# Kernel optimization log

Hardware: AMD Instinct MI355X
Metric: run time of the kernel (lower is better)

The kernel has to match this reference:

```python
import jax, jax.numpy as jnp
import numpy as np

CLASS_W, MASK_W, DICE_W = 1.0, 1.0, 1.0
BIG = 1.0e6


def _hungarian_np(cost):
    """Jonker-Volgenant style shortest-augmenting-path Hungarian (same optimum as
    scipy.optimize.linear_sum_assignment). cost: [R, C] numpy. Returns (row_ind, col_ind)
    with row_ind sorted ascending."""
    C = np.asarray(cost, dtype=np.float64)
    transposed = C.shape[0] > C.shape[1]
    if transposed:
        C = C.T
    n, m = C.shape  # n <= m
    u = np.zeros(n + 1)
    v = np.zeros(m + 1)
    p = np.zeros(m + 1, dtype=np.int64)   # p[j] = row (1-based) matched to col j
    way = np.zeros(m + 1, dtype=np.int64)
    for i in range(1, n + 1):
        p[0] = i
        j0 = 0
        minv = np.full(m + 1, np.inf)
        used = np.zeros(m + 1, dtype=bool)
        while True:
            used[j0] = True
            i0 = p[j0]
            free = ~used
            free[0] = False
            js = np.nonzero(free)[0]
            cur = C[i0 - 1, js - 1] - u[i0] - v[js]
            upd = cur < minv[js]
            minv[js] = np.where(upd, cur, minv[js])
            way[js] = np.where(upd, j0, way[js])
            j1 = js[np.argmin(minv[js])]
            delta = minv[j1]
            u[p[used]] += delta
            v[used] -= delta
            minv[free] -= delta
            j0 = j1
            if p[j0] == 0:
                break
        while j0 != 0:
            j1 = way[j0]
            p[j0] = p[j1]
            j0 = j1
    cols = np.nonzero(p[1:])[0]
    rows = p[1:][cols] - 1
    if transposed:
        rows, cols = cols, rows
    order = np.argsort(rows)
    return rows[order], cols[order]


def _cost_matrix(pred_logits, pred_masks, target_masks, target_labels):
    B, N, H, W = pred_masks.shape
    T = target_labels.shape[1]
    HW = H * W
    # classification cost: -softmax(logits)[..., :-1][:, labels]
    out_prob = jax.nn.softmax(pred_logits, axis=-1)[..., :-1]          # [B, N, C]
    onehot = jax.nn.one_hot(target_labels, out_prob.shape[-1], dtype=out_prob.dtype)  # [B, T, C]
    cost_class = -jnp.einsum('bnc,btc->bnt', out_prob, onehot)
    # nearest-neighbor resize of target masks to pred mask resolution (torch F.interpolate 'nearest')
    Ht, Wt = target_masks.shape[-2:]
    ri = (jnp.arange(H) * Ht) // H
    ci = (jnp.arange(W) * Wt) // W
    tm = target_masks[:, :, ri][:, :, :, ci].reshape(B, T, HW)          # [B, T, HW]
    pm = pred_masks.reshape(B, N, HW)                                    # [B, N, HW]
    # sigmoid BCE cost (vs all-ones/all-zeros decomposition)
    cost_mask = jax.nn.softplus(pm).mean(-1)[:, :, None] - jnp.einsum('bnp,btp->bnt', pm, tm) / HW
    # dice cost
    ps = jax.nn.sigmoid(pm)
    numerator = 2.0 * jnp.einsum('bnp,btp->bnt', ps, tm)
    denominator = ps.sum(-1)[:, :, None] + tm.sum(-1)[:, None, :]
    cost_dice = 1.0 - (numerator + 1.0) / (denominator + 1.0)
    cost = CLASS_W * cost_class + MASK_W * cost_mask + DICE_W * cost_dice
    return jnp.nan_to_num(cost, nan=BIG, posinf=BIG, neginf=-BIG)       # [B, N, T]


_cost_matrix_jit = jax.jit(_cost_matrix)


def setup_inputs() -> dict:
    key = jax.random.key(0)
    k1, k2, k3, k4 = jax.random.split(key, 4)
    pred_logits = jax.random.normal(k1, (8, 100, 81), dtype=jnp.float32)
    pred_masks = jax.random.normal(k2, (8, 100, 256, 256), dtype=jnp.float32)
    target_masks = (jax.random.uniform(k3, (8, 32, 512, 512)) < 0.3).astype(jnp.float32)
    target_labels = jax.random.randint(k4, (8, 32), 0, 80)
    return {
        'pred_logits': pred_logits,
        'pred_masks': pred_masks,
        'target_masks': target_masks,
        'target_labels': target_labels,
    }


def reference(pred_logits, pred_masks, target_masks, target_labels):
    cost = _cost_matrix_jit(pred_logits, pred_masks, target_masks, target_labels)
    costs = np.asarray(cost)  # host sync, mirrors the original .cpu() round-trip
    src_list, tgt_list = [], []
    for b in range(costs.shape[0]):  # serial per-image assignment (inherent to Hungarian)
        r, c = _hungarian_np(costs[b])
        src_list.append(r)
        tgt_list.append(c)
    src = jnp.asarray(np.stack(src_list), dtype=jnp.int64)  # [B, T] query indices
    tgt = jnp.asarray(np.stack(tgt_list), dtype=jnp.int64)  # [B, T] target indices
    return (src, tgt)
```

## Files before the change

### kernel.cpp

```cpp
#include <hip/hip_runtime.h>
#include <stdint.h>


#define BATCH 8
#define NQ    100
#define NT    32
#define HWP   65536
#define NCLS  81
#define BIGV  1.0e6
#define MPAD  112
#define MTILES 7
#define KSPLIT 16
#define KC (HWP / KSPLIT)
#define KW (KC / 4)
#define NITER (KW / 64)

typedef __attribute__((ext_vector_type(8))) short short8;
typedef __attribute__((ext_vector_type(4))) float f32x4;

__device__ inline unsigned short f2bf(float f) {
    uint32_t u = __builtin_bit_cast(uint32_t, f);
    u += 0x7fffu + ((u >> 16) & 1u);
    return (unsigned short)(u >> 16);
}

__global__ __launch_bounds__(256) void pack_kernel(const float* __restrict__ tmask,
                                                   uint32_t* __restrict__ packed,
                                                   int* __restrict__ tm_counts) {
    int idx = blockIdx.x * 256 + threadIdx.x;
    int b = idx >> 16;
    int p = idx & 65535;
    int y = p >> 8, x = p & 255;
    const float* base = tmask + (size_t)b * NT * 262144 + (size_t)(2 * y) * 512 + (2 * x);
    uint32_t w = 0;
#pragma unroll
    for (int t = 0; t < NT; ++t) {
        float v = base[(size_t)t * 262144];
        w |= (v > 0.5f ? 1u : 0u) << t;
    }
    packed[idx] = w;
    int lane = threadIdx.x & 63;
    int mycnt = 0;
#pragma unroll
    for (int t = 0; t < NT; ++t) {
        unsigned long long m = __ballot((w >> t) & 1u);
        if (lane == t) mycnt = __popcll(m);
    }
    if (lane < NT) atomicAdd(&tm_counts[b * NT + lane], mycnt);
}

__global__ __launch_bounds__(256) void mfma_kernel(const float* __restrict__ pmask,
                                                   const uint32_t* __restrict__ packed,
                                                   float* __restrict__ accd,
                                                   float* __restrict__ accs) {
    const int kblk = blockIdx.x;
    const int mt   = blockIdx.y;
    const int b    = blockIdx.z;
    const int tid  = threadIdx.x;
    const int wv   = tid >> 6, lane = tid & 63;
    const int m0   = mt * 16;
    const int q    = lane >> 4;
    const int r    = lane & 15;
    const int kq   = r * 4;

    __shared__ __align__(16) unsigned short Apm[4][16][72];
    __shared__ __align__(16) unsigned short Asg[4][16][72];
    __shared__ __align__(16) unsigned short Bt[4][32][72];
    __shared__ float Cred[8][16][32];

    const float* pmb = pmask + (size_t)b * NQ * HWP;
    const uint32_t* pkb = packed + (size_t)b * HWP;
    const int kbase0 = kblk * KC + wv * KW;

    f32x4 Cpm0 = {0,0,0,0}, Cpm1 = {0,0,0,0}, Csg0 = {0,0,0,0}, Csg1 = {0,0,0,0};
    float rsp[4] = {0,0,0,0}, rsg[4] = {0,0,0,0};

    for (int ki = 0; ki < NITER; ++ki) {
        const int kb = kbase0 + ki * 64;
        float4 vv[4];
#pragma unroll
        for (int L = 0; L < 4; ++L) {
            int m = m0 + L * 4 + q; if (m > NQ - 1) m = NQ - 1;
            vv[L] = *(const float4*)(pmb + (size_t)m * HWP + kb + kq);
        }
        const uint32_t wbits = pkb[kb + lane];
#pragma unroll
        for (int L = 0; L < 4; ++L) {
            const int row = L * 4 + q;
            unsigned short hp[4], hs[4];
#pragma unroll
            for (int e = 0; e < 4; ++e) {
                float pv = (&vv[L].x)[e];
                float ax = fabsf(pv);
                float en = __expf(-ax);
                float inv = __builtin_amdgcn_rcpf(1.0f + en);
                float sig = (pv >= 0.f) ? inv : en * inv;
                float sp  = fmaxf(pv, 0.f) + __logf(1.0f + en);
                rsp[L] += sp; rsg[L] += sig;
                hp[e] = f2bf(pv); hs[e] = f2bf(sig);
            }
            *(uint2*)&Apm[wv][row][kq] = make_uint2(hp[0] | ((uint32_t)hp[1] << 16),
                                                    hp[2] | ((uint32_t)hp[3] << 16));
            *(uint2*)&Asg[wv][row][kq] = make_uint2(hs[0] | ((uint32_t)hs[1] << 16),
                                                    hs[2] | ((uint32_t)hs[3] << 16));
        }
#pragma unroll
        for (int n = 0; n < NT; ++n)
            Bt[wv][n][lane] = ((wbits >> n) & 1u) ? (unsigned short)0x3F80 : (unsigned short)0;
        asm volatile("s_waitcnt lgkmcnt(0)" ::: "memory");
        const short8 a0  = *(const short8*)&Apm[wv][r][q * 8];
        const short8 a1  = *(const short8*)&Apm[wv][r][32 + q * 8];
        const short8 g0  = *(const short8*)&Asg[wv][r][q * 8];
        const short8 g1  = *(const short8*)&Asg[wv][r][32 + q * 8];
        const short8 b00 = *(const short8*)&Bt[wv][r][q * 8];
        const short8 b01 = *(const short8*)&Bt[wv][r][32 + q * 8];
        const short8 b10 = *(const short8*)&Bt[wv][16 + r][q * 8];
        const short8 b11 = *(const short8*)&Bt[wv][16 + r][32 + q * 8];
        Cpm0 = __builtin_amdgcn_mfma_f32_16x16x32_bf16(a0, b00, Cpm0, 0, 0, 0);
        Cpm0 = __builtin_amdgcn_mfma_f32_16x16x32_bf16(a1, b01, Cpm0, 0, 0, 0);
        Cpm1 = __builtin_amdgcn_mfma_f32_16x16x32_bf16(a0, b10, Cpm1, 0, 0, 0);
        Cpm1 = __builtin_amdgcn_mfma_f32_16x16x32_bf16(a1, b11, Cpm1, 0, 0, 0);
        Csg0 = __builtin_amdgcn_mfma_f32_16x16x32_bf16(g0, b00, Csg0, 0, 0, 0);
        Csg0 = __builtin_amdgcn_mfma_f32_16x16x32_bf16(g1, b01, Csg0, 0, 0, 0);
        Csg1 = __builtin_amdgcn_mfma_f32_16x16x32_bf16(g0, b10, Csg1, 0, 0, 0);
        Csg1 = __builtin_amdgcn_mfma_f32_16x16x32_bf16(g1, b11, Csg1, 0, 0, 0);
        asm volatile("" ::: "memory");
    }

#pragma unroll
    for (int e = 0; e < 4; ++e) {
        const int m = q * 4 + e;
        Cred[wv * 2 + 0][m][r]      = Cpm0[e];
        Cred[wv * 2 + 0][m][16 + r] = Cpm1[e];
        Cred[wv * 2 + 1][m][r]      = Csg0[e];
        Cred[wv * 2 + 1][m][16 + r] = Csg1[e];
    }
#pragma unroll
    for (int L = 0; L < 4; ++L) {
#pragma unroll
        for (int s = 8; s > 0; s >>= 1) {
            rsp[L] += __shfl_down(rsp[L], s, 16);
            rsg[L] += __shfl_down(rsg[L], s, 16);
        }
    }
    if (r == 0) {
#pragma unroll
        for (int L = 0; L < 4; ++L) {
            const int m = m0 + L * 4 + q;
            if (m < NQ) {
                atomicAdd(&accs[(size_t)b * MPAD + m], rsp[L]);
                atomicAdd(&accs[(size_t)(BATCH + b) * MPAD + m], rsg[L]);
            }
        }
    }
    __syncthreads();
    for (int idx = tid; idx < 1024; idx += 256) {
        const int type = idx >> 9, rem = idx & 511, m = rem >> 5, n = rem & 31;
        float s = Cred[0 + type][m][n] + Cred[2 + type][m][n]
                + Cred[4 + type][m][n] + Cred[6 + type][m][n];
        const int gm = m0 + m;
        if (gm < NQ)
            atomicAdd(&accd[(size_t)(type * BATCH + b) * MPAD * 32 + (size_t)gm * 32 + n], s);
    }
}

__global__ __launch_bounds__(64) void hungarian_kernel(const float* __restrict__ logits,
                                                       const int* __restrict__ labels,
                                                       const float* __restrict__ accd,
                                                       const float* __restrict__ accs,
                                                       const int* __restrict__ tm_counts,
                                                       int* __restrict__ out) {
    const int b = blockIdx.x;
    const int lane = threadIdx.x;

    __shared__ double Ct[NT][NQ];
    __shared__ double u[NT + 1];
    __shared__ float smx[NQ], ssm[NQ];
    __shared__ float tcs[NT];
    __shared__ int lab[NT];

    if (lane < NT) { tcs[lane] = (float)tm_counts[b * NT + lane]; lab[lane] = labels[b * NT + lane]; }
    for (int n = lane; n < NQ; n += 64) {
        const float* lg = logits + (size_t)(b * NQ + n) * NCLS;
        float mx = -1e30f;
        for (int c = 0; c < NCLS; ++c) mx = fmaxf(mx, lg[c]);
        float s = 0.f;
        for (int c = 0; c < NCLS; ++c) s += __expf(lg[c] - mx);
        smx[n] = mx; ssm[n] = s;
    }
    if (lane <= NT) u[lane] = 0.0;
    __syncthreads();
    for (int idx = lane; idx < NQ * NT; idx += 64) {
        const int t2 = idx & 31, q2 = idx >> 5;
        float dpm = accd[(size_t)b * MPAD * 32 + q2 * 32 + t2];
        float dsg = accd[(size_t)(BATCH + b) * MPAD * 32 + q2 * 32 + t2];
        float ssp = accs[(size_t)b * MPAD + q2];
        float ssg = accs[(size_t)(BATCH + b) * MPAD + q2];
        float lg = logits[(size_t)(b * NQ + q2) * NCLS + lab[t2]];
        float prob = __expf(lg - smx[q2]) / ssm[q2];
        float c = -prob + (ssp - dpm) * (1.0f / (float)HWP)
                + 1.0f - (2.0f * dsg + 1.0f) / (ssg + tcs[t2] + 1.0f);
        if (isnan(c)) c = (float)BIGV;
        else if (isinf(c)) c = (c > 0.f) ? (float)BIGV : -(float)BIGV;
        Ct[t2][q2] = (double)c;
    }
    __syncthreads();

    const int c0 = lane + 1;
    const bool valid1 = (lane < NQ - 64);
    const int c1 = lane + 65;
    const int cidx1 = valid1 ? (lane + 64) : 0;

    double v0 = 0.0, v1 = 0.0;
    int p0 = 0, p1 = 0;

    for (int i = 1; i <= NT; ++i) {
        double minv0 = 1e300, minv1 = 1e300;
        int way0 = 0, way1 = 0;
        bool used0 = false, used1 = !valid1;
        double du0 = 0.0, du1 = 0.0, dtot = 0.0;
        int j0 = 0, i0 = i;
        int jfin = 0;

        for (int guard = 0; guard < 160; ++guard) {
            double u_i0 = u[i0];
            double cur0 = Ct[i0 - 1][lane] - u_i0 - v0;
            if (!used0 && cur0 < minv0) { minv0 = cur0; way0 = j0; }
            double cur1 = Ct[i0 - 1][cidx1] - u_i0 - v1;
            if (!used1 && cur1 < minv1) { minv1 = cur1; way1 = j0; }
            double bv = 1e301; int bj = 1 << 20;
            if (!used0) { bv = minv0; bj = c0; }
            if (!used1 && minv1 < bv) { bv = minv1; bj = c1; }
#pragma unroll
            for (int s = 32; s > 0; s >>= 1) {
                double ov = __shfl_down(bv, s, 64);
                int    oj = __shfl_down(bj, s, 64);
                if (ov < bv || (ov == bv && oj < bj)) { bv = ov; bj = oj; }
            }
            double delta = __shfl(bv, 0, 64);
            int j1 = __shfl(bj, 0, 64);
            dtot += delta;
            if (used0) { v0 -= delta; du0 += delta; } else { minv0 -= delta; }
            if (valid1) {
                if (used1) { v1 -= delta; du1 += delta; } else { minv1 -= delta; }
            }
            if (c0 == j1) used0 = true;
            if (valid1 && c1 == j1) used1 = true;
            int src = (j1 - 1) & 63, slot = (j1 - 1) >> 6;
            int pa = __shfl(p0, src, 64), pb = __shfl(p1, src, 64);
            int pj1 = slot ? pb : pa;
            if (pj1 == 0) { jfin = j1; break; }
            j0 = j1; i0 = pj1;
        }

        if (used0 && p0 != 0) u[p0] += du0;
        if (valid1 && used1 && p1 != 0) u[p1] += du1;
        if (lane == 0) u[i] += dtot;

        int jj = jfin;
        for (int guard = 0; guard < 160 && jj != 0; ++guard) {
            int src = (jj - 1) & 63, slot = (jj - 1) >> 6;
            int wa = __shfl(way0, src, 64), wb = __shfl(way1, src, 64);
            int jprev = slot ? wb : wa;
            int pnew;
            if (jprev == 0) pnew = i;
            else {
                int s2 = (jprev - 1) & 63, sl2 = (jprev - 1) >> 6;
                int pa = __shfl(p0, s2, 64), pb = __shfl(p1, s2, 64);
                pnew = sl2 ? pb : pa;
            }
            if (c0 == jj) p0 = pnew;
            if (valid1 && c1 == jj) p1 = pnew;
            jj = jprev;
        }
        __syncthreads();
    }

    unsigned long long m0 = __ballot(p0 != 0);
    unsigned long long m1 = __ballot(valid1 && p1 != 0);
    int base = b * NT;
    if (p0 != 0) {
        int rank = __popcll(m0 & ((1ull << lane) - 1ull));
        out[base + rank] = c0 - 1;
        out[BATCH * NT + base + rank] = p0 - 1;
    }
    if (valid1 && p1 != 0) {
        int rank = __popcll(m0) + __popcll(m1 & ((1ull << lane) - 1ull));
        out[base + rank] = c1 - 1;
        out[BATCH * NT + base + rank] = p1 - 1;
    }
}

extern "C" void kernel_launch(void* const* d_in, const int* in_sizes, int n_in,
                              void* d_out, int out_size, void* d_ws, size_t ws_size,
                              hipStream_t stream) {
    const float* logits = (const float*)d_in[0];
    const float* pmasks = (const float*)d_in[1];
    const float* tmasks = (const float*)d_in[2];
    const int*   labels = (const int*)d_in[3];

    uint8_t* ws = (uint8_t*)d_ws;
    uint32_t* packed = (uint32_t*)ws;
    uint8_t* zbase = ws + (size_t)BATCH * HWP * 4;
    int* tm_counts = (int*)zbase;
    float* accd = (float*)(zbase + 1024);
    float* accs = (float*)(zbase + 1024 + 229376);
    const size_t ztotal = 1024 + 229376 + 7168;

    int* out = (int*)d_out;

    hipMemsetAsync(zbase, 0, ztotal, stream);
    pack_kernel<<<BATCH * HWP / 256, 256, 0, stream>>>(tmasks, packed, tm_counts);
    mfma_kernel<<<dim3(KSPLIT, MTILES, BATCH), 256, 0, stream>>>(pmasks, packed, accd, accs);
    hungarian_kernel<<<BATCH, 64, 0, stream>>>(logits, labels, accd, accs, tm_counts, out);
}
```

Measured before the change: 605.9 us.

## Build MFMA operands directly in registers and cache Hungarian duals in registers

The dice/mask MFMA kernel no longer stages the converted bf16 prediction tiles and expanded target-bit tiles through LDS. Each lane now loads exactly the prediction elements and packed target words it needs for its MFMA fragment, converts them in registers, and reduces the per-row softplus/sigmoid sums with two cross-lane shuffles. This removes the LDS writes, reads and waits on every iteration. In exchange, the packed target words are loaded redundantly across lanes, and the global access pattern for the prediction rows changes. The Hungarian kernel also reads the row potential u through a wave shuffle from a register copy refreshed once per row, rather than from shared memory on every augmenting step.

```diff
diff --git a/kernel.cpp b/kernel.cpp
--- a/kernel.cpp
+++ b/kernel.cpp
@@ -61,61 +61,65 @@
     const int m0   = mt * 16;
     const int q    = lane >> 4;
     const int r    = lane & 15;
-    const int kq   = r * 4;
-
-    __shared__ __align__(16) unsigned short Apm[4][16][72];
-    __shared__ __align__(16) unsigned short Asg[4][16][72];
-    __shared__ __align__(16) unsigned short Bt[4][32][72];
+
     __shared__ float Cred[8][16][32];
 
-    const float* pmb = pmask + (size_t)b * NQ * HWP;
+    int mrow = m0 + r; if (mrow > NQ - 1) mrow = NQ - 1;
+    const float* Arow = pmask + (size_t)b * NQ * HWP + (size_t)mrow * HWP;
     const uint32_t* pkb = packed + (size_t)b * HWP;
     const int kbase0 = kblk * KC + wv * KW;
 
     f32x4 Cpm0 = {0,0,0,0}, Cpm1 = {0,0,0,0}, Csg0 = {0,0,0,0}, Csg1 = {0,0,0,0};
-    float rsp[4] = {0,0,0,0}, rsg[4] = {0,0,0,0};
+    float rsp = 0.f, rsg = 0.f;
 
     for (int ki = 0; ki < NITER; ++ki) {
         const int kb = kbase0 + ki * 64;
-        float4 vv[4];
-#pragma unroll
-        for (int L = 0; L < 4; ++L) {
-            int m = m0 + L * 4 + q; if (m > NQ - 1) m = NQ - 1;
-            vv[L] = *(const float4*)(pmb + (size_t)m * HWP + kb + kq);
-        }
-        const uint32_t wbits = pkb[kb + lane];
-#pragma unroll
-        for (int L = 0; L < 4; ++L) {
-            const int row = L * 4 + q;
-            unsigned short hp[4], hs[4];
+        const float4 va0 = *(const float4*)(Arow + kb + q * 8);
+        const float4 va1 = *(const float4*)(Arow + kb + q * 8 + 4);
+        const float4 va2 = *(const float4*)(Arow + kb + 32 + q * 8);
+        const float4 va3 = *(const float4*)(Arow + kb + 32 + q * 8 + 4);
+        const uint4  wb0 = *(const uint4*)(pkb + kb + q * 8);
+        const uint4  wb1 = *(const uint4*)(pkb + kb + q * 8 + 4);
+        const uint4  wb2 = *(const uint4*)(pkb + kb + 32 + q * 8);
+        const uint4  wb3 = *(const uint4*)(pkb + kb + 32 + q * 8 + 4);
+
+        short8 a0, a1, g0, g1;
+        auto cvt4 = [&](const float4& v, short8& af, short8& gf, int base) {
 #pragma unroll
             for (int e = 0; e < 4; ++e) {
-                float pv = (&vv[L].x)[e];
+                float pv = (&v.x)[e];
                 float ax = fabsf(pv);
                 float en = __expf(-ax);
                 float inv = __builtin_amdgcn_rcpf(1.0f + en);
                 float sig = (pv >= 0.f) ? inv : en * inv;
                 float sp  = fmaxf(pv, 0.f) + __logf(1.0f + en);
-                rsp[L] += sp; rsg[L] += sig;
-                hp[e] = f2bf(pv); hs[e] = f2bf(sig);
+                rsp += sp; rsg += sig;
+                af[base + e] = (short)f2bf(pv);
+                gf[base + e] = (short)f2bf(sig);
             }
-            *(uint2*)&Apm[wv][row][kq] = make_uint2(hp[0] | ((uint32_t)hp[1] << 16),
-                                                    hp[2] | ((uint32_t)hp[3] << 16));
-            *(uint2*)&Asg[wv][row][kq] = make_uint2(hs[0] | ((uint32_t)hs[1] << 16),
-                                                    hs[2] | ((uint32_t)hs[3] << 16));
+        };
+        cvt4(va0, a0, g0, 0); cvt4(va1, a0, g0, 4);
+        cvt4(va2, a1, g1, 0); cvt4(va3, a1, g1, 4);
+
+        short8 b00, b01, b10, b11;
+        const unsigned short ONE = 0x3F80;
+#pragma unroll
+        for (int j = 0; j < 4; ++j) {
+            uint32_t s;
+            s = (&wb0.x)[j] >> r;
+            b00[j]     = (short)((s & 1u)         ? ONE : 0);
+            b10[j]     = (short)(((s >> 16) & 1u) ? ONE : 0);
+            s = (&wb1.x)[j] >> r;
+            b00[4 + j] = (short)((s & 1u)         ? ONE : 0);
+            b10[4 + j] = (short)(((s >> 16) & 1u) ? ONE : 0);
+            s = (&wb2.x)[j] >> r;
+            b01[j]     = (short)((s & 1u)         ? ONE : 0);
+            b11[j]     = (short)(((s >> 16) & 1u) ? ONE : 0);
+            s = (&wb3.x)[j] >> r;
+            b01[4 + j] = (short)((s & 1u)         ? ONE : 0);
+            b11[4 + j] = (short)(((s >> 16) & 1u) ? ONE : 0);
         }
-#pragma unroll
-        for (int n = 0; n < NT; ++n)
-            Bt[wv][n][lane] = ((wbits >> n) & 1u) ? (unsigned short)0x3F80 : (unsigned short)0;
-        asm volatile("s_waitcnt lgkmcnt(0)" ::: "memory");
-        const short8 a0  = *(const short8*)&Apm[wv][r][q * 8];
-        const short8 a1  = *(const short8*)&Apm[wv][r][32 + q * 8];
-        const short8 g0  = *(const short8*)&Asg[wv][r][q * 8];
-        const short8 g1  = *(const short8*)&Asg[wv][r][32 + q * 8];
-        const short8 b00 = *(const short8*)&Bt[wv][r][q * 8];
-        const short8 b01 = *(const short8*)&Bt[wv][r][32 + q * 8];
-        const short8 b10 = *(const short8*)&Bt[wv][16 + r][q * 8];
-        const short8 b11 = *(const short8*)&Bt[wv][16 + r][32 + q * 8];
+
         Cpm0 = __builtin_amdgcn_mfma_f32_16x16x32_bf16(a0, b00, Cpm0, 0, 0, 0);
         Cpm0 = __builtin_amdgcn_mfma_f32_16x16x32_bf16(a1, b01, Cpm0, 0, 0, 0);
         Cpm1 = __builtin_amdgcn_mfma_f32_16x16x32_bf16(a0, b10, Cpm1, 0, 0, 0);
@@ -124,7 +128,15 @@
         Csg0 = __builtin_amdgcn_mfma_f32_16x16x32_bf16(g1, b01, Csg0, 0, 0, 0);
         Csg1 = __builtin_amdgcn_mfma_f32_16x16x32_bf16(g0, b10, Csg1, 0, 0, 0);
         Csg1 = __builtin_amdgcn_mfma_f32_16x16x32_bf16(g1, b11, Csg1, 0, 0, 0);
-        asm volatile("" ::: "memory");
+    }
+
+    rsp += __shfl_xor(rsp, 16, 64);
+    rsp += __shfl_xor(rsp, 32, 64);
+    rsg += __shfl_xor(rsg, 16, 64);
+    rsg += __shfl_xor(rsg, 32, 64);
+    if (q == 0 && m0 + r < NQ) {
+        atomicAdd(&accs[(size_t)b * MPAD + m0 + r], rsp);
+        atomicAdd(&accs[(size_t)(BATCH + b) * MPAD + m0 + r], rsg);
     }
 
 #pragma unroll
@@ -134,24 +146,6 @@
         Cred[wv * 2 + 0][m][16 + r] = Cpm1[e];
         Cred[wv * 2 + 1][m][r]      = Csg0[e];
         Cred[wv * 2 + 1][m][16 + r] = Csg1[e];
-    }
-#pragma unroll
-    for (int L = 0; L < 4; ++L) {
-#pragma unroll
-        for (int s = 8; s > 0; s >>= 1) {
-            rsp[L] += __shfl_down(rsp[L], s, 16);
-            rsg[L] += __shfl_down(rsg[L], s, 16);
-        }
-    }
-    if (r == 0) {
-#pragma unroll
-        for (int L = 0; L < 4; ++L) {
-            const int m = m0 + L * 4 + q;
-            if (m < NQ) {
-                atomicAdd(&accs[(size_t)b * MPAD + m], rsp[L]);
-                atomicAdd(&accs[(size_t)(BATCH + b) * MPAD + m], rsg[L]);
-            }
-        }
     }
     __syncthreads();
     for (int idx = tid; idx < 1024; idx += 256) {
@@ -213,6 +207,7 @@
 
     double v0 = 0.0, v1 = 0.0;
     int p0 = 0, p1 = 0;
+    double u_reg = 0.0;
 
     for (int i = 1; i <= NT; ++i) {
         double minv0 = 1e300, minv1 = 1e300;
@@ -223,7 +218,7 @@
         int jfin = 0;
 
         for (int guard = 0; guard < 160; ++guard) {
-            double u_i0 = u[i0];
+            double u_i0 = __shfl(u_reg, i0, 64);
             double cur0 = Ct[i0 - 1][lane] - u_i0 - v0;
             if (!used0 && cur0 < minv0) { minv0 = cur0; way0 = j0; }
             double cur1 = Ct[i0 - 1][cidx1] - u_i0 - v1;
@@ -274,6 +269,7 @@
             jj = jprev;
         }
         __syncthreads();
+        u_reg = (lane <= NT) ? u[lane] : 0.0;
     }
 
     unsigned long long m0 = __ballot(p0 != 0);
```

New measurement: 598.6 us. No clear change (-1.2%).
